# Kernel optimization log

Hardware: AMD Instinct MI355X
Metric: run time of the kernel (lower is better)

## Reference

```python
import jax, jax.numpy as jnp
import numpy as np

CD_W = 0.2  # chamfer_weight
EPS = 1e-7


def setup_inputs() -> dict:
    key = jax.random.key(0)
    k1, k2, k3, k4, k5 = jax.random.split(key, 5)
    B, N, K = 16, 4096, 4096
    num_add, obj_num_p = 8, 512
    return {
        "adv_pc": jax.random.normal(k1, (B, N, 3), dtype=jnp.float32),
        "ori_pc": jax.random.normal(k2, (B, K, 3), dtype=jnp.float32),
        "adv_obj": jax.random.normal(k3, (B, num_add, obj_num_p, 3), dtype=jnp.float32),
        "ori_obj": jax.random.normal(k4, (B, num_add, obj_num_p, 3), dtype=jnp.float32),
        "weights": jax.random.uniform(k5, (B,), dtype=jnp.float32),
    }


def reference(adv_pc, ori_pc, adv_obj, ori_obj, weights):
    B = adv_pc.shape[0]
    # --- Chamfer (method='adv2ori'): mean over adv points of min squared dist to ori ---
    a2 = jnp.sum(adv_pc * adv_pc, axis=-1)            # [B, N]
    o2 = jnp.sum(ori_pc * ori_pc, axis=-1)            # [B, K]
    cross = jnp.einsum('bnd,bkd->bnk', adv_pc, ori_pc)  # [B, N, K]
    sqdist = a2[:, :, None] + o2[:, None, :] - 2.0 * cross  # [B, N, K]
    loss1 = jnp.mean(jnp.min(sqdist, axis=2), axis=1)  # [B] adv->ori NN sq dist
    chamfer_loss = jnp.mean(loss1 * weights)
    # --- Global L2 dist between flattened adv/ori objects ---
    diff = adv_obj.reshape(B, -1, 3) - ori_obj.reshape(B, -1, 3)
    l2 = jnp.sqrt(jnp.sum(diff * diff, axis=(1, 2)) + EPS)  # [B]
    l2_loss = jnp.mean(l2 * weights)
    return l2_loss + CD_W * chamfer_loss
```

## Files before the change

### kernel.cpp

```cpp
#include <hip/hip_runtime.h>
#include <math.h>

typedef short bf16x8 __attribute__((ext_vector_type(8)));
typedef float f32x16 __attribute__((ext_vector_type(16)));
typedef unsigned int u32x4 __attribute__((ext_vector_type(4)));

#define B 16
#define N 4096
#define K 4096
#define OBJ_ELEMS (8*512*3)
#define OBJ_VEC4  (OBJ_ELEMS/4)
#define NSEG 32
#define NCHUNK (N/NSEG)
#define BLK 512
#define OBJ_V4_PER_BLK (OBJ_VEC4/NSEG)
#define CD_W 0.2f
#define EPS_F 1e-7f

#define CS_OFF 0
#define LS_OFF (B*NSEG)

__device__ __forceinline__ unsigned short f2bf(float f) {
    unsigned int u = __float_as_uint(f);
    u = (u + 0x7FFFu + ((u >> 16) & 1u)) >> 16;
    return (unsigned short)u;
}

__global__ __launch_bounds__(BLK) void chamfer_mfma_kernel(
    const float* __restrict__ adv, const float* __restrict__ ori,
    const float* __restrict__ adv_obj, const float* __restrict__ ori_obj,
    float* __restrict__ csum, float* __restrict__ lsq)
{
    __shared__ ushort4 slds[K];
    __shared__ float   rowmin[8][32];
    __shared__ float   a2lds[NCHUNK];
    __shared__ float   red_c[2], red_l[2];

    const int nseg = blockIdx.x;
    const int b    = blockIdx.y;
    const int tid  = threadIdx.x;
    const int wid  = tid >> 6;
    const int lane = tid & 63;
    const int col  = lane & 31;
    const int hi   = lane >> 5;
    const int rg   = wid & 3;
    const int kh   = wid >> 2;

    #pragma unroll
    for (int i = 0; i < K/BLK; ++i) {
        int p = tid + i*BLK;
        const float* s = ori + (b*K + p)*3;
        float x = s[0], y = s[1], z = s[2];
        float o2 = x*x + y*y + z*z;
        ushort4 u;
        u.x = f2bf(-2.f*x); u.y = f2bf(-2.f*y);
        u.z = f2bf(-2.f*z); u.w = f2bf(o2);
        slds[p] = u;
    }

    const int n = nseg*NCHUNK + rg*32 + col;
    const float* ap = adv + (b*N + n)*3;
    float ax = ap[0], ay = ap[1], az = ap[2];
    float a2 = ax*ax + ay*ay + az*az;
    if (kh == 0 && hi == 0) a2lds[rg*32 + col] = a2;
    bf16x8 afrag;
    if (hi == 0) {
        afrag[0] = (short)f2bf(ax);
        afrag[1] = (short)f2bf(ay);
        afrag[2] = (short)f2bf(az);
        afrag[3] = (short)0x3F80;
    } else {
        afrag[0] = 0; afrag[1] = 0; afrag[2] = 0; afrag[3] = 0;
    }
    afrag[4] = 0; afrag[5] = 0; afrag[6] = 0; afrag[7] = 0;

    __syncthreads();

    f32x16 acc = {INFINITY,INFINITY,INFINITY,INFINITY,
                  INFINITY,INFINITY,INFINITY,INFINITY,
                  INFINITY,INFINITY,INFINITY,INFINITY,
                  INFINITY,INFINITY,INFINITY,INFINITY};
    const f32x16 zc = {0,0,0,0, 0,0,0,0, 0,0,0,0, 0,0,0,0};
    const uint2* s2 = reinterpret_cast<const uint2*>(slds);

    #pragma unroll 4
    for (int t = kh*64; t < kh*64 + 64; t += 2) {
        uint2 q0 = s2[t*32 + col];
        uint2 q1 = s2[(t+1)*32 + col];
        u32x4 w0 = {q0.x, q0.y, 0u, 0u};
        u32x4 w1 = {q1.x, q1.y, 0u, 0u};
        bf16x8 b0 = __builtin_bit_cast(bf16x8, w0);
        bf16x8 b1 = __builtin_bit_cast(bf16x8, w1);
        f32x16 c0 = __builtin_amdgcn_mfma_f32_32x32x16_bf16(afrag, b0, zc, 0,0,0);
        f32x16 c1 = __builtin_amdgcn_mfma_f32_32x32x16_bf16(afrag, b1, zc, 0,0,0);
        #pragma unroll
        for (int r = 0; r < 16; ++r)
            acc[r] = fminf(fminf(c0[r], c1[r]), acc[r]);
    }

    #pragma unroll
    for (int r = 0; r < 16; ++r) {
        float v = acc[r];
        v = fminf(v, __shfl_xor(v, 1));
        v = fminf(v, __shfl_xor(v, 2));
        v = fminf(v, __shfl_xor(v, 4));
        v = fminf(v, __shfl_xor(v, 8));
        v = fminf(v, __shfl_xor(v, 16));
        acc[r] = v;
    }
    if (col == 0) {
        #pragma unroll
        for (int r = 0; r < 16; ++r)
            rowmin[wid][(r&3) + 8*(r>>2) + 4*hi] = acc[r];
    }
    __syncthreads();

    float s = 0.f;
    if (wid < 2) {
        int row = tid;
        int rg2 = row >> 5, ri = row & 31;
        float m = fminf(rowmin[rg2][ri], rowmin[4 + rg2][ri]);
        s = m + a2lds[row];
    } else if (wid < 4) {
        int li = (wid - 2)*64 + lane;
        if (li < OBJ_V4_PER_BLK) {
            int idx = b*OBJ_VEC4 + nseg*OBJ_V4_PER_BLK + li;
            float4 a = reinterpret_cast<const float4*>(adv_obj)[idx];
            float4 o = reinterpret_cast<const float4*>(ori_obj)[idx];
            float dx = a.x - o.x, dy = a.y - o.y, dz = a.z - o.z, dw = a.w - o.w;
            s = dx*dx + dy*dy + dz*dz + dw*dw;
        }
    }
    #pragma unroll
    for (int off = 32; off; off >>= 1) s += __shfl_down(s, off);
    if (lane == 0) {
        if (wid < 2)       red_c[wid]     = s;
        else if (wid < 4)  red_l[wid - 2] = s;
    }
    __syncthreads();
    if (tid == 0) csum[b*NSEG + nseg] = red_c[0] + red_c[1];
    if (tid == 1) lsq [b*NSEG + nseg] = red_l[0] + red_l[1];
}

__global__ __launch_bounds__(256) void final_kernel(
    const float* __restrict__ csum, const float* __restrict__ lsq,
    const float* __restrict__ w, float* __restrict__ out)
{
    const int tid = threadIdx.x;
    float c = csum[2*tid] + csum[2*tid + 1];
    float l = lsq [2*tid] + lsq [2*tid + 1];
    #pragma unroll
    for (int off = 8; off; off >>= 1) {
        c += __shfl_down(c, off, 16);
        l += __shfl_down(l, off, 16);
    }
    __shared__ float sc[B], sl[B];
    int bb = tid >> 4;
    if ((tid & 15) == 0) { sc[bb] = c; sl[bb] = l; }
    __syncthreads();
    if (tid < 64) {
        float cc = 0.f, ll = 0.f;
        if (tid < B) {
            float wt = w[tid];
            cc = (sc[tid] / (float)N) * wt;
            ll = sqrtf(sl[tid] + EPS_F) * wt;
        }
        #pragma unroll
        for (int off = 8; off; off >>= 1) {
            cc += __shfl_down(cc, off);
            ll += __shfl_down(ll, off);
        }
        if (tid == 0) out[0] = ll / (float)B + CD_W * (cc / (float)B);
    }
}

extern "C" void kernel_launch(void* const* d_in, const int* in_sizes, int n_in,
                              void* d_out, int out_size, void* d_ws, size_t ws_size,
                              hipStream_t stream)
{
    const float* adv_pc  = (const float*)d_in[0];
    const float* ori_pc  = (const float*)d_in[1];
    const float* adv_obj = (const float*)d_in[2];
    const float* ori_obj = (const float*)d_in[3];
    const float* weights = (const float*)d_in[4];
    float* out = (float*)d_out;
    float* ws  = (float*)d_ws;

    float* csum = ws + CS_OFF;
    float* lsq  = ws + LS_OFF;

    chamfer_mfma_kernel<<<dim3(NSEG, B), dim3(BLK), 0, stream>>>(
        adv_pc, ori_pc, adv_obj, ori_obj, csum, lsq);

    final_kernel<<<dim3(1), dim3(256), 0, stream>>>(csum, lsq, weights, out);
}
```

Measured before the change: 19.69 us.

## Fuse final reduction via last-block atomic counter and widen LDS loads

```diff
diff --git a/kernel.cpp b/kernel.cpp
--- a/kernel.cpp
+++ b/kernel.cpp
@@ -13,12 +13,14 @@
 #define NSEG 32
 #define NCHUNK (N/NSEG)
 #define BLK 512
+#define NBLOCKS (NSEG*B)
 #define OBJ_V4_PER_BLK (OBJ_VEC4/NSEG)
 #define CD_W 0.2f
 #define EPS_F 1e-7f
 
 #define CS_OFF 0
-#define LS_OFF (B*NSEG)
+#define LS_OFF NBLOCKS
+#define CNT_OFF (2*NBLOCKS)
 
 __device__ __forceinline__ unsigned short f2bf(float f) {
     unsigned int u = __float_as_uint(f);
@@ -26,15 +28,19 @@
     return (unsigned short)u;
 }
 
-__global__ __launch_bounds__(BLK) void chamfer_mfma_kernel(
+__global__ __launch_bounds__(BLK) void chamfer_fused_kernel(
     const float* __restrict__ adv, const float* __restrict__ ori,
     const float* __restrict__ adv_obj, const float* __restrict__ ori_obj,
-    float* __restrict__ csum, float* __restrict__ lsq)
+    const float* __restrict__ w,
+    float* __restrict__ csum, float* __restrict__ lsq, int* __restrict__ cnt,
+    float* __restrict__ out)
 {
     __shared__ ushort4 slds[K];
     __shared__ float   rowmin[8][32];
     __shared__ float   a2lds[NCHUNK];
     __shared__ float   red_c[2], red_l[2];
+    __shared__ int     lastflag;
+    __shared__ float   sc[B], sl[B];
 
     const int nseg = blockIdx.x;
     const int b    = blockIdx.y;
@@ -81,14 +87,14 @@
                   INFINITY,INFINITY,INFINITY,INFINITY,
                   INFINITY,INFINITY,INFINITY,INFINITY};
     const f32x16 zc = {0,0,0,0, 0,0,0,0, 0,0,0,0, 0,0,0,0};
-    const uint2* s2 = reinterpret_cast<const uint2*>(slds);
+    const float4* s4 = reinterpret_cast<const float4*>(slds);
 
     #pragma unroll 4
-    for (int t = kh*64; t < kh*64 + 64; t += 2) {
-        uint2 q0 = s2[t*32 + col];
-        uint2 q1 = s2[(t+1)*32 + col];
-        u32x4 w0 = {q0.x, q0.y, 0u, 0u};
-        u32x4 w1 = {q1.x, q1.y, 0u, 0u};
+    for (int it = kh*32; it < kh*32 + 32; ++it) {
+        float4 q = s4[it*32 + col];
+        u32x4 uu = __builtin_bit_cast(u32x4, q);
+        u32x4 w0 = {uu.x, uu.y, 0u, 0u};
+        u32x4 w1 = {uu.z, uu.w, 0u, 0u};
         bf16x8 b0 = __builtin_bit_cast(bf16x8, w0);
         bf16x8 b1 = __builtin_bit_cast(bf16x8, w1);
         f32x16 c0 = __builtin_amdgcn_mfma_f32_32x32x16_bf16(afrag, b0, zc, 0,0,0);
@@ -138,25 +144,29 @@
         else if (wid < 4)  red_l[wid - 2] = s;
     }
     __syncthreads();
-    if (tid == 0) csum[b*NSEG + nseg] = red_c[0] + red_c[1];
-    if (tid == 1) lsq [b*NSEG + nseg] = red_l[0] + red_l[1];
-}
-
-__global__ __launch_bounds__(256) void final_kernel(
-    const float* __restrict__ csum, const float* __restrict__ lsq,
-    const float* __restrict__ w, float* __restrict__ out)
-{
-    const int tid = threadIdx.x;
-    float c = csum[2*tid] + csum[2*tid + 1];
-    float l = lsq [2*tid] + lsq [2*tid + 1];
-    #pragma unroll
-    for (int off = 8; off; off >>= 1) {
-        c += __shfl_down(c, off, 16);
-        l += __shfl_down(l, off, 16);
-    }
-    __shared__ float sc[B], sl[B];
-    int bb = tid >> 4;
-    if ((tid & 15) == 0) { sc[bb] = c; sl[bb] = l; }
+
+    if (tid == 0) {
+        csum[b*NSEG + nseg] = red_c[0] + red_c[1];
+        lsq [b*NSEG + nseg] = red_l[0] + red_l[1];
+        __threadfence();
+        int old = atomicAdd(cnt, 1);
+        lastflag = (old == NBLOCKS - 1);
+    }
+    __syncthreads();
+    if (!lastflag) return;
+
+    __threadfence();
+    {
+        float c = csum[tid];
+        float l = lsq [tid];
+        #pragma unroll
+        for (int off = 16; off; off >>= 1) {
+            c += __shfl_down(c, off, 32);
+            l += __shfl_down(l, off, 32);
+        }
+        int bb = tid >> 5;
+        if ((tid & 31) == 0) { sc[bb] = c; sl[bb] = l; }
+    }
     __syncthreads();
     if (tid < 64) {
         float cc = 0.f, ll = 0.f;
@@ -188,9 +198,10 @@
 
     float* csum = ws + CS_OFF;
     float* lsq  = ws + LS_OFF;
-
-    chamfer_mfma_kernel<<<dim3(NSEG, B), dim3(BLK), 0, stream>>>(
-        adv_pc, ori_pc, adv_obj, ori_obj, csum, lsq);
-
-    final_kernel<<<dim3(1), dim3(256), 0, stream>>>(csum, lsq, weights, out);
+    int*   cnt  = (int*)(ws + CNT_OFF);
+
+    hipMemsetAsync(cnt, 0, sizeof(int), stream);
+
+    chamfer_fused_kernel<<<dim3(NSEG, B), dim3(BLK), 0, stream>>>(
+        adv_pc, ori_pc, adv_obj, ori_obj, weights, csum, lsq, cnt, out);
 }
```

Result: slower. 31.60 us (+60.5%).
